# Optimization experiments

Hardware: AMD Instinct MI355X
Metric: run time of the kernel (lower is better)

## Reference

```python
import jax, jax.numpy as jnp
import numpy as np

B, C, T = 128, 8, 128   # batch, channels, time steps
K, S = 20, 128          # known classes, barycenter length


def setup_inputs() -> dict:
    key = jax.random.key(0)
    k1, k2, k3, k4, k5 = jax.random.split(key, 5)
    x = jax.random.normal(k1, (B, C, T), dtype=jnp.float32)
    preds = jax.random.randint(k2, (B,), 0, K).astype(jnp.int32)
    barycenters = jax.random.normal(k3, (K, S, C), dtype=jnp.float32)
    # thresholds centered near realistic scales so both detector branches fire
    top_dist = 7.0 + 0.5 * jax.random.normal(k4, (K,), dtype=jnp.float32)
    bottom_cc = 25.0 + 5.0 * jax.random.normal(k5, (K, C), dtype=jnp.float32)
    return {"x": x, "preds": preds, "barycenters": barycenters,
            "top_dist": top_dist, "bottom_cc": bottom_cc}


def _dtw_dist(cost):
    """Classic DTW DP over a [T, S] sq-euclidean cost matrix; returns accumulated cost."""
    inf = jnp.asarray(jnp.inf, cost.dtype)
    row0 = jnp.cumsum(cost[0])  # first row: only left moves

    def row_step(prev, crow):
        prev_shift = jnp.concatenate([jnp.full((1,), inf, cost.dtype), prev[:-1]])
        def col_step(left, inp):
            c, p, ps = inp
            v = c + jnp.minimum(jnp.minimum(p, ps), left)
            return v, v
        _, row = jax.lax.scan(col_step, inf, (crow, prev, prev_shift))
        return row, None

    last, _ = jax.lax.scan(row_step, row0, cost[1:])
    return last[-1]


def reference(x, preds, barycenters, top_dist, bottom_cc):
    xt = jnp.transpose(x, (0, 2, 1))                    # [B, T, C]
    x2 = jnp.sum(xt * xt, axis=-1)                      # [B, T]
    b2 = jnp.sum(barycenters * barycenters, axis=-1)    # [K, S]
    dots = jnp.einsum('btc,ksc->bkts', xt, barycenters)  # [B, K, T, S]
    cost = jnp.maximum(x2[:, None, :, None] + b2[None, :, None, :] - 2.0 * dots, 0.0)

    Bn, Kn, Tn, Sn = cost.shape
    dists = jax.vmap(_dtw_dist)(cost.reshape(Bn * Kn, Tn, Sn)).reshape(Bn, Kn)
    log_dists = jnp.log(dists)
    dtw_unknown = jnp.all(log_dists > top_dist[None, :], axis=1)   # [B]

    # per-channel full cross-correlation max vs each barycenter
    corr_max = lambda a, v: jnp.max(jnp.correlate(a, v, mode='full'))
    per_ch = jax.vmap(corr_max, in_axes=(1, 1))          # over channels -> [C]
    per_cls = jax.vmap(per_ch, in_axes=(None, 0))        # over classes  -> [K, C]
    per_b = jax.vmap(per_cls, in_axes=(0, None))         # over batch    -> [B, K, C]
    ccs = per_b(xt, barycenters)
    # class 'fails' if any channel cc is not above its bottom threshold
    cc_unknown = jnp.all(jnp.any(ccs <= bottom_cc[None, :, :], axis=2), axis=1)  # [B]

    unknown = cc_unknown | dtw_unknown
    return jnp.where(unknown, Kn, preds)
```

## Files before the change

kernel.cpp:

```cpp
#include <hip/hip_runtime.h>
#include <hip/hip_bf16.h>
#include <math.h>

#define B_ 128
#define C_ 8
#define T_ 128
#define K_ 20
#define S_ 128

__global__ __launch_bounds__(64) void dtw_kernel(const float* __restrict__ x,
                                                 const float* __restrict__ bary,
                                                 const float* __restrict__ top_dist,
                                                 int* __restrict__ dtw_gt) {
    int pair = blockIdx.x;
    int b = pair / K_;
    int kk = pair - b * K_;
    int lane = threadIdx.x;

    __shared__ __align__(16) float xs[T_][C_];

    #pragma unroll
    for (int i = 0; i < (T_ * C_) / 64; ++i) {
        int idx = i * 64 + lane;
        int t = idx & (T_ - 1);
        int c = idx >> 7;
        xs[t][c] = x[(b * C_ + c) * T_ + t];
    }

    float bv0[8], bv1[8];
    {
        const float4* bp = (const float4*)(bary + (size_t)(kk * S_ + 2 * lane) * C_);
        float4 a0 = bp[0], a1 = bp[1], a2 = bp[2], a3 = bp[3];
        bv0[0] = a0.x; bv0[1] = a0.y; bv0[2] = a0.z; bv0[3] = a0.w;
        bv0[4] = a1.x; bv0[5] = a1.y; bv0[6] = a1.z; bv0[7] = a1.w;
        bv1[0] = a2.x; bv1[1] = a2.y; bv1[2] = a2.z; bv1[3] = a2.w;
        bv1[4] = a3.x; bv1[5] = a3.y; bv1[6] = a3.z; bv1[7] = a3.w;
    }
    __syncthreads();

    const float INF = __builtin_inff();
    float c0 = INF, c1 = INF, p0 = INF, p1 = INF;

    for (int d = 0; d < T_ + 63; ++d) {
        float lc = __shfl_up(c1, 1);
        float lp = __shfl_up(p1, 1);
        int t = d - lane;
        if (t >= 0 && t < T_) {
            p0 = c0;
            p1 = c1;
            float4 xa = *(const float4*)&xs[t][0];
            float4 xb = *(const float4*)&xs[t][4];
            float xv[8];
            xv[0] = xa.x; xv[1] = xa.y; xv[2] = xa.z; xv[3] = xa.w;
            xv[4] = xb.x; xv[5] = xb.y; xv[6] = xb.z; xv[7] = xb.w;
            float cost0 = 0.0f, cost1 = 0.0f;
            #pragma unroll
            for (int ch = 0; ch < 8; ++ch) {
                float d0 = xv[ch] - bv0[ch];
                float d1 = xv[ch] - bv1[ch];
                cost0 = fmaf(d0, d0, cost0);
                cost1 = fmaf(d1, d1, cost1);
            }
            float up0 = (t == 0) ? INF : p0;
            float up1 = (t == 0) ? INF : p1;
            float dg1 = (t == 0) ? INF : p0;
            float dg0, lf0;
            if (lane == 0) {
                dg0 = (t == 0) ? 0.0f : INF;
                lf0 = INF;
            } else {
                dg0 = (t == 0) ? INF : lp;
                lf0 = lc;
            }
            c0 = cost0 + fminf(fminf(up0, dg0), lf0);
            c1 = cost1 + fminf(fminf(up1, dg1), c0);
        }
    }

    if (lane == 63) {
        dtw_gt[pair] = (logf(c1) > top_dist[kk]) ? 1 : 0;
    }
}

#define CC_ROW 396

__global__ __launch_bounds__(256) void cc_kernel(const float* __restrict__ x,
                                                 const float* __restrict__ bary,
                                                 const float* __restrict__ bottom_cc,
                                                 int* __restrict__ cc_fail) {
    int pair = blockIdx.x;
    int b = pair / K_;
    int kk = pair - b * K_;
    int tid = threadIdx.x;

    __shared__ __align__(16) float xp[C_ * CC_ROW];
    __shared__ __align__(16) float bt[C_][S_];
    __shared__ int fail;

    if (tid == 0) fail = 0;

    for (int i = tid; i < C_ * CC_ROW; i += 256) {
        int c = i / CC_ROW;
        int j = i - c * CC_ROW;
        int t = j - (S_ - 1);
        float v = 0.0f;
        if (t >= 0 && t < T_) v = x[(b * C_ + c) * T_ + t];
        xp[i] = v;
    }
    for (int i = tid; i < C_ * S_; i += 256) {
        int s = i >> 3;
        int c = i & 7;
        bt[c][s] = bary[(kk * S_ + s) * C_ + c];
    }
    __syncthreads();

    int c = tid >> 5;
    int l = tid & 31;
    int lag0 = l * 8;
    const float* xr = &xp[c * CC_ROW];

    float w[12];
    #pragma unroll
    for (int i = 0; i < 12; i += 4) {
        float4 v4 = *(const float4*)(xr + lag0 + i);
        w[i] = v4.x; w[i + 1] = v4.y; w[i + 2] = v4.z; w[i + 3] = v4.w;
    }
    float acc[8] = {0.f, 0.f, 0.f, 0.f, 0.f, 0.f, 0.f, 0.f};

    for (int s4 = 0; s4 < S_; s4 += 4) {
        #pragma unroll
        for (int u = 0; u < 4; ++u) {
            float bval = bt[c][s4 + u];
            #pragma unroll
            for (int j = 0; j < 8; ++j)
                acc[j] = fmaf(w[u + j], bval, acc[j]);
        }
        #pragma unroll
        for (int i = 0; i < 8; ++i) w[i] = w[i + 4];
        float4 v4 = *(const float4*)(xr + lag0 + s4 + 12);
        w[8] = v4.x; w[9] = v4.y; w[10] = v4.z; w[11] = v4.w;
    }

    if (l == 31) acc[7] = -__builtin_inff();
    float m = acc[0];
    #pragma unroll
    for (int j = 1; j < 8; ++j) m = fmaxf(m, acc[j]);
    #pragma unroll
    for (int off = 16; off > 0; off >>= 1)
        m = fmaxf(m, __shfl_xor(m, off));

    if (l == 0) {
        if (m <= bottom_cc[kk * C_ + c]) atomicOr(&fail, 1);
    }
    __syncthreads();
    if (tid == 0) cc_fail[pair] = fail;
}

__global__ void final_kernel(const int* __restrict__ preds,
                             const int* __restrict__ dtw_gt,
                             const int* __restrict__ cc_fail,
                             int* __restrict__ out) {
    int b = threadIdx.x;
    if (b < B_) {
        int dtw_all = 1, cc_all = 1;
        #pragma unroll
        for (int k = 0; k < K_; ++k) {
            dtw_all &= dtw_gt[b * K_ + k];
            cc_all &= cc_fail[b * K_ + k];
        }
        out[b] = (dtw_all | cc_all) ? K_ : preds[b];
    }
}

extern "C" void kernel_launch(void* const* d_in, const int* in_sizes, int n_in,
                              void* d_out, int out_size, void* d_ws, size_t ws_size,
                              hipStream_t stream) {
    const float* x         = (const float*)d_in[0];
    const int*   preds     = (const int*)d_in[1];
    const float* bary      = (const float*)d_in[2];
    const float* top_dist  = (const float*)d_in[3];
    const float* bottom_cc = (const float*)d_in[4];
    int* out = (int*)d_out;

    int* dtw_gt  = (int*)d_ws;
    int* cc_fail = dtw_gt + B_ * K_;

    dtw_kernel<<<B_ * K_, 64, 0, stream>>>(x, bary, top_dist, dtw_gt);
    cc_kernel<<<B_ * K_, 256, 0, stream>>>(x, bary, bottom_cc, cc_fail);
    final_kernel<<<1, 128, 0, stream>>>(preds, dtw_gt, cc_fail, out);
}
```

Baseline: 65.20 us.

## Fuse DTW and cross-correlation kernels into one interleaved launch

Merges the DTW and cross-correlation kernels into a single 3200-block launch. Every fifth block runs four DTW pairs, one per wave, and the other blocks each run one CC pair, so the two workloads overlap on the GPU and one launch is dropped. The DTW cost is now computed as |x|^2+|b|^2-2x·b using precomputed norms and pre-scaled barycenter values, matching the reference formula. The wavefront loop is simplified with clamped indexing and a carried left-diagonal value, which removes one shuffle per step. The CC inner loop is fully unrolled.

```diff
diff --git a/kernel.cpp b/kernel.cpp
--- a/kernel.cpp
+++ b/kernel.cpp
@@ -8,152 +8,188 @@
 #define K_ 20
 #define S_ 128
 
-__global__ __launch_bounds__(64) void dtw_kernel(const float* __restrict__ x,
-                                                 const float* __restrict__ bary,
-                                                 const float* __restrict__ top_dist,
-                                                 int* __restrict__ dtw_gt) {
-    int pair = blockIdx.x;
-    int b = pair / K_;
-    int kk = pair - b * K_;
-    int lane = threadIdx.x;
-
-    __shared__ __align__(16) float xs[T_][C_];
-
-    #pragma unroll
-    for (int i = 0; i < (T_ * C_) / 64; ++i) {
-        int idx = i * 64 + lane;
-        int t = idx & (T_ - 1);
-        int c = idx >> 7;
-        xs[t][c] = x[(b * C_ + c) * T_ + t];
+#define CC_ROW 396
+#define DTW_TILE_F 1152
+#define SMEM_BYTES 18816
+
+__global__ __launch_bounds__(256) void fused_kernel(const float* __restrict__ x,
+                                                    const float* __restrict__ bary,
+                                                    const float* __restrict__ top_dist,
+                                                    const float* __restrict__ bottom_cc,
+                                                    int* __restrict__ dtw_gt,
+                                                    int* __restrict__ cc_fail) {
+    __shared__ __align__(16) unsigned char smem[SMEM_BYTES];
+    int u = blockIdx.x;
+    int tid = threadIdx.x;
+
+    if (u % 5 == 0) {
+        int wave = tid >> 6;
+        int lane = tid & 63;
+        int pair = (u / 5) * 4 + wave;
+        int b = pair / K_;
+        int kk = pair - b * K_;
+        float* tile = (float*)smem + wave * DTW_TILE_F;
+
+        #pragma unroll
+        for (int i = 0; i < 16; ++i) {
+            int idx = i * 64 + lane;
+            int c = idx >> 7;
+            int t = idx & 127;
+            float v = x[(b * C_ + c) * T_ + t];
+            tile[t * 4 + (c & 3) + ((c >> 2) * 512)] = v;
+        }
+        __syncthreads();
+        #pragma unroll
+        for (int rep = 0; rep < 2; ++rep) {
+            int t = rep * 64 + lane;
+            float4 xa = *(const float4*)&tile[t * 4];
+            float4 xb = *(const float4*)&tile[512 + t * 4];
+            float s = xa.x * xa.x;
+            s = fmaf(xa.y, xa.y, s); s = fmaf(xa.z, xa.z, s); s = fmaf(xa.w, xa.w, s);
+            s = fmaf(xb.x, xb.x, s); s = fmaf(xb.y, xb.y, s); s = fmaf(xb.z, xb.z, s);
+            s = fmaf(xb.w, xb.w, s);
+            tile[1024 + t] = s;
+        }
+        __syncthreads();
+
+        float bv0[8], bv1[8], B20, B21;
+        {
+            const float4* bp = (const float4*)(bary + (size_t)(kk * S_ + 2 * lane) * C_);
+            float4 q0 = bp[0], q1 = bp[1], q2 = bp[2], q3 = bp[3];
+            bv0[0]=q0.x; bv0[1]=q0.y; bv0[2]=q0.z; bv0[3]=q0.w;
+            bv0[4]=q1.x; bv0[5]=q1.y; bv0[6]=q1.z; bv0[7]=q1.w;
+            bv1[0]=q2.x; bv1[1]=q2.y; bv1[2]=q2.z; bv1[3]=q2.w;
+            bv1[4]=q3.x; bv1[5]=q3.y; bv1[6]=q3.z; bv1[7]=q3.w;
+            float s0 = 0.f, s1 = 0.f;
+            #pragma unroll
+            for (int ch = 0; ch < 8; ++ch) {
+                s0 = fmaf(bv0[ch], bv0[ch], s0);
+                s1 = fmaf(bv1[ch], bv1[ch], s1);
+            }
+            B20 = s0; B21 = s1;
+            #pragma unroll
+            for (int ch = 0; ch < 8; ++ch) { bv0[ch] *= -2.f; bv1[ch] *= -2.f; }
+        }
+
+        const float INF = __builtin_inff();
+        float c0 = INF, c1 = INF, lcp = INF;
+        bool is0 = (lane == 0);
+
+        if (is0) {
+            float bse = tile[1024];
+            float4 xa = *(const float4*)&tile[0];
+            float4 xb = *(const float4*)&tile[512];
+            float a0 = bse + B20, a1 = bse + B21;
+            a0 = fmaf(bv0[0], xa.x, a0); a0 = fmaf(bv0[1], xa.y, a0);
+            a0 = fmaf(bv0[2], xa.z, a0); a0 = fmaf(bv0[3], xa.w, a0);
+            a0 = fmaf(bv0[4], xb.x, a0); a0 = fmaf(bv0[5], xb.y, a0);
+            a0 = fmaf(bv0[6], xb.z, a0); a0 = fmaf(bv0[7], xb.w, a0);
+            a1 = fmaf(bv1[0], xa.x, a1); a1 = fmaf(bv1[1], xa.y, a1);
+            a1 = fmaf(bv1[2], xa.z, a1); a1 = fmaf(bv1[3], xa.w, a1);
+            a1 = fmaf(bv1[4], xb.x, a1); a1 = fmaf(bv1[5], xb.y, a1);
+            a1 = fmaf(bv1[6], xb.z, a1); a1 = fmaf(bv1[7], xb.w, a1);
+            c0 = fmaxf(a0, 0.f);
+            c1 = fmaxf(a1, 0.f) + c0;
+        }
+
+        for (int d = 1; d < T_ + 63; ++d) {
+            float lcs = __shfl_up(c1, 1);
+            float lc = is0 ? INF : lcs;
+            int t = d - lane;
+            if (t >= 0) {
+                int tc = (t < 127) ? t : 127;
+                float bse = tile[1024 + tc];
+                float4 xa = *(const float4*)&tile[tc * 4];
+                float4 xb = *(const float4*)&tile[512 + tc * 4];
+                float a0 = bse + B20, a1 = bse + B21;
+                a0 = fmaf(bv0[0], xa.x, a0); a0 = fmaf(bv0[1], xa.y, a0);
+                a0 = fmaf(bv0[2], xa.z, a0); a0 = fmaf(bv0[3], xa.w, a0);
+                a0 = fmaf(bv0[4], xb.x, a0); a0 = fmaf(bv0[5], xb.y, a0);
+                a0 = fmaf(bv0[6], xb.z, a0); a0 = fmaf(bv0[7], xb.w, a0);
+                a1 = fmaf(bv1[0], xa.x, a1); a1 = fmaf(bv1[1], xa.y, a1);
+                a1 = fmaf(bv1[2], xa.z, a1); a1 = fmaf(bv1[3], xa.w, a1);
+                a1 = fmaf(bv1[4], xb.x, a1); a1 = fmaf(bv1[5], xb.y, a1);
+                a1 = fmaf(bv1[6], xb.z, a1); a1 = fmaf(bv1[7], xb.w, a1);
+                a0 = fmaxf(a0, 0.f);
+                a1 = fmaxf(a1, 0.f);
+                float n0 = a0 + fminf(fminf(c0, lcp), lc);
+                float n1 = a1 + fminf(fminf(c1, c0), n0);
+                c0 = n0; c1 = n1;
+            }
+            lcp = lc;
+        }
+
+        if (lane == 63)
+            dtw_gt[pair] = (logf(c1) > top_dist[kk]) ? 1 : 0;
+    } else {
+        int pair = u - (u + 4) / 5;
+        int b = pair / K_;
+        int kk = pair - b * K_;
+
+        float* xp = (float*)smem;
+        float* bt = xp + C_ * CC_ROW;
+        int* fail = (int*)(bt + C_ * S_);
+
+        if (tid == 0) *fail = 0;
+
+        for (int i = tid; i < C_ * CC_ROW; i += 256) {
+            int c = i / CC_ROW;
+            int j = i - c * CC_ROW;
+            int t = j - (S_ - 1);
+            float v = 0.0f;
+            if (t >= 0 && t < T_) v = x[(b * C_ + c) * T_ + t];
+            xp[i] = v;
+        }
+        for (int i = tid; i < C_ * S_; i += 256) {
+            int s = i >> 3;
+            int c = i & 7;
+            bt[c * S_ + s] = bary[(kk * S_ + s) * C_ + c];
+        }
+        __syncthreads();
+
+        int c = tid >> 5;
+        int l = tid & 31;
+        int lag0 = l * 8;
+        const float* xr = &xp[c * CC_ROW];
+        const float* br = &bt[c * S_];
+
+        float w[12];
+        #pragma unroll
+        for (int i = 0; i < 12; i += 4) {
+            float4 v4 = *(const float4*)(xr + lag0 + i);
+            w[i] = v4.x; w[i+1] = v4.y; w[i+2] = v4.z; w[i+3] = v4.w;
+        }
+        float acc[8] = {0.f,0.f,0.f,0.f,0.f,0.f,0.f,0.f};
+
+        #pragma unroll
+        for (int s4 = 0; s4 < S_; s4 += 4) {
+            #pragma unroll
+            for (int uu = 0; uu < 4; ++uu) {
+                float bval = br[s4 + uu];
+                #pragma unroll
+                for (int j = 0; j < 8; ++j)
+                    acc[j] = fmaf(w[uu + j], bval, acc[j]);
+            }
+            #pragma unroll
+            for (int i = 0; i < 8; ++i) w[i] = w[i + 4];
+            float4 v4 = *(const float4*)(xr + lag0 + s4 + 12);
+            w[8] = v4.x; w[9] = v4.y; w[10] = v4.z; w[11] = v4.w;
+        }
+
+        if (l == 31) acc[7] = -__builtin_inff();
+        float m = acc[0];
+        #pragma unroll
+        for (int j = 1; j < 8; ++j) m = fmaxf(m, acc[j]);
+        #pragma unroll
+        for (int off = 16; off > 0; off >>= 1)
+            m = fmaxf(m, __shfl_xor(m, off));
+
+        if (l == 0) {
+            if (m <= bottom_cc[kk * C_ + c]) atomicOr(fail, 1);
+        }
+        __syncthreads();
+        if (tid == 0) cc_fail[pair] = *fail;
     }
-
-    float bv0[8], bv1[8];
-    {
-        const float4* bp = (const float4*)(bary + (size_t)(kk * S_ + 2 * lane) * C_);
-        float4 a0 = bp[0], a1 = bp[1], a2 = bp[2], a3 = bp[3];
-        bv0[0] = a0.x; bv0[1] = a0.y; bv0[2] = a0.z; bv0[3] = a0.w;
-        bv0[4] = a1.x; bv0[5] = a1.y; bv0[6] = a1.z; bv0[7] = a1.w;
-        bv1[0] = a2.x; bv1[1] = a2.y; bv1[2] = a2.z; bv1[3] = a2.w;
-        bv1[4] = a3.x; bv1[5] = a3.y; bv1[6] = a3.z; bv1[7] = a3.w;
-    }
-    __syncthreads();
-
-    const float INF = __builtin_inff();
-    float c0 = INF, c1 = INF, p0 = INF, p1 = INF;
-
-    for (int d = 0; d < T_ + 63; ++d) {
-        float lc = __shfl_up(c1, 1);
-        float lp = __shfl_up(p1, 1);
-        int t = d - lane;
-        if (t >= 0 && t < T_) {
-            p0 = c0;
-            p1 = c1;
-            float4 xa = *(const float4*)&xs[t][0];
-            float4 xb = *(const float4*)&xs[t][4];
-            float xv[8];
-            xv[0] = xa.x; xv[1] = xa.y; xv[2] = xa.z; xv[3] = xa.w;
-            xv[4] = xb.x; xv[5] = xb.y; xv[6] = xb.z; xv[7] = xb.w;
-            float cost0 = 0.0f, cost1 = 0.0f;
-            #pragma unroll
-            for (int ch = 0; ch < 8; ++ch) {
-                float d0 = xv[ch] - bv0[ch];
-                float d1 = xv[ch] - bv1[ch];
-                cost0 = fmaf(d0, d0, cost0);
-                cost1 = fmaf(d1, d1, cost1);
-            }
-            float up0 = (t == 0) ? INF : p0;
-            float up1 = (t == 0) ? INF : p1;
-            float dg1 = (t == 0) ? INF : p0;
-            float dg0, lf0;
-            if (lane == 0) {
-                dg0 = (t == 0) ? 0.0f : INF;
-                lf0 = INF;
-            } else {
-                dg0 = (t == 0) ? INF : lp;
-                lf0 = lc;
-            }
-            c0 = cost0 + fminf(fminf(up0, dg0), lf0);
-            c1 = cost1 + fminf(fminf(up1, dg1), c0);
-        }
-    }
-
-    if (lane == 63) {
-        dtw_gt[pair] = (logf(c1) > top_dist[kk]) ? 1 : 0;
-    }
-}
-
-#define CC_ROW 396
-
-__global__ __launch_bounds__(256) void cc_kernel(const float* __restrict__ x,
-                                                 const float* __restrict__ bary,
-                                                 const float* __restrict__ bottom_cc,
-                                                 int* __restrict__ cc_fail) {
-    int pair = blockIdx.x;
-    int b = pair / K_;
-    int kk = pair - b * K_;
-    int tid = threadIdx.x;
-
-    __shared__ __align__(16) float xp[C_ * CC_ROW];
-    __shared__ __align__(16) float bt[C_][S_];
-    __shared__ int fail;
-
-    if (tid == 0) fail = 0;
-
-    for (int i = tid; i < C_ * CC_ROW; i += 256) {
-        int c = i / CC_ROW;
-        int j = i - c * CC_ROW;
-        int t = j - (S_ - 1);
-        float v = 0.0f;
-        if (t >= 0 && t < T_) v = x[(b * C_ + c) * T_ + t];
-        xp[i] = v;
-    }
-    for (int i = tid; i < C_ * S_; i += 256) {
-        int s = i >> 3;
-        int c = i & 7;
-        bt[c][s] = bary[(kk * S_ + s) * C_ + c];
-    }
-    __syncthreads();
-
-    int c = tid >> 5;
-    int l = tid & 31;
-    int lag0 = l * 8;
-    const float* xr = &xp[c * CC_ROW];
-
-    float w[12];
-    #pragma unroll
-    for (int i = 0; i < 12; i += 4) {
-        float4 v4 = *(const float4*)(xr + lag0 + i);
-        w[i] = v4.x; w[i + 1] = v4.y; w[i + 2] = v4.z; w[i + 3] = v4.w;
-    }
-    float acc[8] = {0.f, 0.f, 0.f, 0.f, 0.f, 0.f, 0.f, 0.f};
-
-    for (int s4 = 0; s4 < S_; s4 += 4) {
-        #pragma unroll
-        for (int u = 0; u < 4; ++u) {
-            float bval = bt[c][s4 + u];
-            #pragma unroll
-            for (int j = 0; j < 8; ++j)
-                acc[j] = fmaf(w[u + j], bval, acc[j]);
-        }
-        #pragma unroll
-        for (int i = 0; i < 8; ++i) w[i] = w[i + 4];
-        float4 v4 = *(const float4*)(xr + lag0 + s4 + 12);
-        w[8] = v4.x; w[9] = v4.y; w[10] = v4.z; w[11] = v4.w;
-    }
-
-    if (l == 31) acc[7] = -__builtin_inff();
-    float m = acc[0];
-    #pragma unroll
-    for (int j = 1; j < 8; ++j) m = fmaxf(m, acc[j]);
-    #pragma unroll
-    for (int off = 16; off > 0; off >>= 1)
-        m = fmaxf(m, __shfl_xor(m, off));
-
-    if (l == 0) {
-        if (m <= bottom_cc[kk * C_ + c]) atomicOr(&fail, 1);
-    }
-    __syncthreads();
-    if (tid == 0) cc_fail[pair] = fail;
 }
 
 __global__ void final_kernel(const int* __restrict__ preds,
@@ -185,7 +221,6 @@
     int* dtw_gt  = (int*)d_ws;
     int* cc_fail = dtw_gt + B_ * K_;
 
-    dtw_kernel<<<B_ * K_, 64, 0, stream>>>(x, bary, top_dist, dtw_gt);
-    cc_kernel<<<B_ * K_, 256, 0, stream>>>(x, bary, bottom_cc, cc_fail);
+    fused_kernel<<<3200, 256, 0, stream>>>(x, bary, top_dist, bottom_cc, dtw_gt, cc_fail);
     final_kernel<<<1, 128, 0, stream>>>(preds, dtw_gt, cc_fail, out);
 }
```

New measurement: 76.09 us. 1.17x slower.

## Fuse DTW and cross-correlation into one interleaved heterogeneous-block kernel

Applied to the files above, without the earlier changes.

Merges the DTW and cross-correlation kernels into a single launch of 6400 single-wave blocks. One in five blocks runs DTW for two classes using 32 lanes each with four columns per lane, which shortens the wavefront diagonal. The DTW cost is computed from precomputed norms plus a dot product. The remaining blocks each handle half the channels of a (batch, class) pair for cross-correlation, with a 16-lag register window and a swizzled shared layout. The intent is to overlap the latency-bound DTW chains with FMA-heavy correlation work and to cut launch overhead, at the cost of more registers and uneven block durations.

```diff
diff --git a/kernel.cpp b/kernel.cpp
--- a/kernel.cpp
+++ b/kernel.cpp
@@ -8,157 +8,188 @@
 #define K_ 20
 #define S_ 128
 
-__global__ __launch_bounds__(64) void dtw_kernel(const float* __restrict__ x,
-                                                 const float* __restrict__ bary,
-                                                 const float* __restrict__ top_dist,
-                                                 int* __restrict__ dtw_gt) {
-    int pair = blockIdx.x;
-    int b = pair / K_;
-    int kk = pair - b * K_;
+#define XROW 384
+#define BTROW 132
+#define SWZ(j) ((j) ^ ((((j) >> 5) & 7) << 2))
+#define SMEMF 2080
+
+__global__ __launch_bounds__(64) void fused_kernel(const float* __restrict__ x,
+                                                   const float* __restrict__ bary,
+                                                   const float* __restrict__ top_dist,
+                                                   const float* __restrict__ bottom_cc,
+                                                   int* __restrict__ dtw_gt,
+                                                   int* __restrict__ cc_fail2) {
+    __shared__ __align__(16) float smem[SMEMF];
+    const float INF = __builtin_inff();
+    int u = blockIdx.x;
     int lane = threadIdx.x;
 
-    __shared__ __align__(16) float xs[T_][C_];
-
-    #pragma unroll
-    for (int i = 0; i < (T_ * C_) / 64; ++i) {
-        int idx = i * 64 + lane;
-        int t = idx & (T_ - 1);
-        int c = idx >> 7;
-        xs[t][c] = x[(b * C_ + c) * T_ + t];
-    }
-
-    float bv0[8], bv1[8];
-    {
-        const float4* bp = (const float4*)(bary + (size_t)(kk * S_ + 2 * lane) * C_);
-        float4 a0 = bp[0], a1 = bp[1], a2 = bp[2], a3 = bp[3];
-        bv0[0] = a0.x; bv0[1] = a0.y; bv0[2] = a0.z; bv0[3] = a0.w;
-        bv0[4] = a1.x; bv0[5] = a1.y; bv0[6] = a1.z; bv0[7] = a1.w;
-        bv1[0] = a2.x; bv1[1] = a2.y; bv1[2] = a2.z; bv1[3] = a2.w;
-        bv1[4] = a3.x; bv1[5] = a3.y; bv1[6] = a3.z; bv1[7] = a3.w;
-    }
-    __syncthreads();
-
-    const float INF = __builtin_inff();
-    float c0 = INF, c1 = INF, p0 = INF, p1 = INF;
-
-    for (int d = 0; d < T_ + 63; ++d) {
-        float lc = __shfl_up(c1, 1);
-        float lp = __shfl_up(p1, 1);
-        int t = d - lane;
-        if (t >= 0 && t < T_) {
-            p0 = c0;
-            p1 = c1;
-            float4 xa = *(const float4*)&xs[t][0];
-            float4 xb = *(const float4*)&xs[t][4];
-            float xv[8];
-            xv[0] = xa.x; xv[1] = xa.y; xv[2] = xa.z; xv[3] = xa.w;
-            xv[4] = xb.x; xv[5] = xb.y; xv[6] = xb.z; xv[7] = xb.w;
-            float cost0 = 0.0f, cost1 = 0.0f;
+    if (u % 5 == 0) {
+        int w = u / 5;
+        int b = w / 10;
+        int j2 = w - b * 10;
+        int gl = lane & 31;
+        int kk = j2 * 2 + (lane >> 5);
+
+        #pragma unroll
+        for (int i = 0; i < 4; ++i) {
+            int vid = i * 64 + lane;
+            int c = vid >> 5;
+            int t0 = (vid & 31) << 2;
+            float4 v = *(const float4*)(x + ((size_t)b * C_ + c) * T_ + t0);
+            float* dst = &smem[(c >> 2) * 512 + (c & 3)];
+            dst[(t0 + 0) * 4] = v.x;
+            dst[(t0 + 1) * 4] = v.y;
+            dst[(t0 + 2) * 4] = v.z;
+            dst[(t0 + 3) * 4] = v.w;
+        }
+        __syncthreads();
+        #pragma unroll
+        for (int r = 0; r < 2; ++r) {
+            int t = r * 64 + lane;
+            float4 xa = *(const float4*)&smem[t * 4];
+            float4 xb = *(const float4*)&smem[512 + t * 4];
+            float s = xa.x * xa.x;
+            s = fmaf(xa.y, xa.y, s); s = fmaf(xa.z, xa.z, s); s = fmaf(xa.w, xa.w, s);
+            s = fmaf(xb.x, xb.x, s); s = fmaf(xb.y, xb.y, s); s = fmaf(xb.z, xb.z, s);
+            s = fmaf(xb.w, xb.w, s);
+            smem[1024 + t] = s;
+        }
+        __syncthreads();
+
+        float bv[4][8], B2s[4];
+        {
+            const float4* bp = (const float4*)(bary + ((size_t)kk * S_ + 4 * gl) * C_);
             #pragma unroll
-            for (int ch = 0; ch < 8; ++ch) {
-                float d0 = xv[ch] - bv0[ch];
-                float d1 = xv[ch] - bv1[ch];
-                cost0 = fmaf(d0, d0, cost0);
-                cost1 = fmaf(d1, d1, cost1);
-            }
-            float up0 = (t == 0) ? INF : p0;
-            float up1 = (t == 0) ? INF : p1;
-            float dg1 = (t == 0) ? INF : p0;
-            float dg0, lf0;
-            if (lane == 0) {
-                dg0 = (t == 0) ? 0.0f : INF;
-                lf0 = INF;
-            } else {
-                dg0 = (t == 0) ? INF : lp;
-                lf0 = lc;
-            }
-            c0 = cost0 + fminf(fminf(up0, dg0), lf0);
-            c1 = cost1 + fminf(fminf(up1, dg1), c0);
-        }
-    }
-
-    if (lane == 63) {
-        dtw_gt[pair] = (logf(c1) > top_dist[kk]) ? 1 : 0;
+            for (int r = 0; r < 4; ++r) {
+                float4 q0 = bp[2 * r], q1 = bp[2 * r + 1];
+                bv[r][0] = q0.x; bv[r][1] = q0.y; bv[r][2] = q0.z; bv[r][3] = q0.w;
+                bv[r][4] = q1.x; bv[r][5] = q1.y; bv[r][6] = q1.z; bv[r][7] = q1.w;
+                float s = 0.f;
+                #pragma unroll
+                for (int ch = 0; ch < 8; ++ch) s = fmaf(bv[r][ch], bv[r][ch], s);
+                B2s[r] = s;
+                #pragma unroll
+                for (int ch = 0; ch < 8; ++ch) bv[r][ch] *= -2.f;
+            }
+        }
+
+        bool is0 = (gl == 0);
+        float cr0 = INF, cr1 = INF, cr2 = INF, cr3 = INF;
+        float lcp = is0 ? 0.f : INF;
+
+        for (int d = 0; d < T_ + 31; ++d) {
+            float lcs = __shfl_up(cr3, 1);
+            float lc = is0 ? INF : lcs;
+            int t = d - gl;
+            if (t >= 0) {
+                int tc = (t < T_ - 1) ? t : (T_ - 1);
+                float bse = smem[1024 + tc];
+                float4 xa = *(const float4*)&smem[tc * 4];
+                float4 xb = *(const float4*)&smem[512 + tc * 4];
+                float xv[8];
+                xv[0] = xa.x; xv[1] = xa.y; xv[2] = xa.z; xv[3] = xa.w;
+                xv[4] = xb.x; xv[5] = xb.y; xv[6] = xb.z; xv[7] = xb.w;
+                float a0 = bse + B2s[0], a1 = bse + B2s[1];
+                float a2 = bse + B2s[2], a3 = bse + B2s[3];
+                #pragma unroll
+                for (int ch = 0; ch < 8; ++ch) {
+                    a0 = fmaf(bv[0][ch], xv[ch], a0);
+                    a1 = fmaf(bv[1][ch], xv[ch], a1);
+                    a2 = fmaf(bv[2][ch], xv[ch], a2);
+                    a3 = fmaf(bv[3][ch], xv[ch], a3);
+                }
+                a0 = fmaxf(a0, 0.f); a1 = fmaxf(a1, 0.f);
+                a2 = fmaxf(a2, 0.f); a3 = fmaxf(a3, 0.f);
+                float n0 = a0 + fminf(fminf(cr0, lcp), lc);
+                float n1 = a1 + fminf(fminf(cr1, cr0), n0);
+                float n2 = a2 + fminf(fminf(cr2, cr1), n1);
+                float n3 = a3 + fminf(fminf(cr3, cr2), n2);
+                cr0 = n0; cr1 = n1; cr2 = n2; cr3 = n3;
+            }
+            lcp = lc;
+        }
+
+        if (gl == 31)
+            dtw_gt[b * K_ + kk] = (logf(cr3) > top_dist[kk]) ? 1 : 0;
+    } else {
+        int idx = u - u / 5 - 1;
+        int pair = idx >> 1;
+        int h = idx & 1;
+        int b = pair / K_;
+        int kk = pair - b * K_;
+        int cbase = h * 4;
+
+        float* xp = smem;
+        float* bt = smem + 4 * XROW;
+
+        #pragma unroll
+        for (int c = 0; c < 4; ++c)
+            for (int j = lane; j < XROW; j += 64) {
+                int t = j - (S_ - 1);
+                float v = 0.f;
+                if (t >= 0 && t < T_) v = x[((size_t)b * C_ + cbase + c) * T_ + t];
+                xp[c * XROW + SWZ(j)] = v;
+            }
+        for (int i = lane; i < 4 * S_; i += 64) {
+            int s = i >> 2, c = i & 3;
+            bt[c * BTROW + s] = bary[((size_t)kk * S_ + s) * C_ + cbase + c];
+        }
+        __syncthreads();
+
+        int cl = lane >> 4;
+        int gl = lane & 15;
+        int lag0 = gl << 4;
+        const float* xr = xp + cl * XROW;
+        const float* br = bt + cl * BTROW;
+
+        float wdw[20];
+        #pragma unroll
+        for (int i = 0; i < 5; ++i) {
+            float4 v = *(const float4*)&xr[SWZ(lag0 + i * 4)];
+            wdw[i * 4 + 0] = v.x; wdw[i * 4 + 1] = v.y;
+            wdw[i * 4 + 2] = v.z; wdw[i * 4 + 3] = v.w;
+        }
+        float acc[16];
+        #pragma unroll
+        for (int j = 0; j < 16; ++j) acc[j] = 0.f;
+
+        #pragma unroll
+        for (int s4 = 0; s4 < S_; s4 += 4) {
+            float4 bq = *(const float4*)&br[s4];
+            float bvals[4] = {bq.x, bq.y, bq.z, bq.w};
+            #pragma unroll
+            for (int uu = 0; uu < 4; ++uu) {
+                #pragma unroll
+                for (int j = 0; j < 16; ++j)
+                    acc[j] = fmaf(wdw[uu + j], bvals[uu], acc[j]);
+            }
+            if (s4 < S_ - 4) {
+                #pragma unroll
+                for (int i = 0; i < 16; ++i) wdw[i] = wdw[i + 4];
+                float4 v = *(const float4*)&xr[SWZ(lag0 + s4 + 20)];
+                wdw[16] = v.x; wdw[17] = v.y; wdw[18] = v.z; wdw[19] = v.w;
+            }
+        }
+
+        if (gl == 15) acc[15] = -INF;
+        float m = acc[0];
+        #pragma unroll
+        for (int j = 1; j < 16; ++j) m = fmaxf(m, acc[j]);
+        #pragma unroll
+        for (int off = 8; off >= 1; off >>= 1)
+            m = fmaxf(m, __shfl_xor(m, off));
+
+        bool fail = false;
+        if (gl == 0) fail = (m <= bottom_cc[kk * C_ + cbase + cl]);
+        unsigned long long bal = __ballot(fail);
+        if (lane == 0) cc_fail2[pair * 2 + h] = (bal != 0ULL) ? 1 : 0;
     }
 }
 
-#define CC_ROW 396
-
-__global__ __launch_bounds__(256) void cc_kernel(const float* __restrict__ x,
-                                                 const float* __restrict__ bary,
-                                                 const float* __restrict__ bottom_cc,
-                                                 int* __restrict__ cc_fail) {
-    int pair = blockIdx.x;
-    int b = pair / K_;
-    int kk = pair - b * K_;
-    int tid = threadIdx.x;
-
-    __shared__ __align__(16) float xp[C_ * CC_ROW];
-    __shared__ __align__(16) float bt[C_][S_];
-    __shared__ int fail;
-
-    if (tid == 0) fail = 0;
-
-    for (int i = tid; i < C_ * CC_ROW; i += 256) {
-        int c = i / CC_ROW;
-        int j = i - c * CC_ROW;
-        int t = j - (S_ - 1);
-        float v = 0.0f;
-        if (t >= 0 && t < T_) v = x[(b * C_ + c) * T_ + t];
-        xp[i] = v;
-    }
-    for (int i = tid; i < C_ * S_; i += 256) {
-        int s = i >> 3;
-        int c = i & 7;
-        bt[c][s] = bary[(kk * S_ + s) * C_ + c];
-    }
-    __syncthreads();
-
-    int c = tid >> 5;
-    int l = tid & 31;
-    int lag0 = l * 8;
-    const float* xr = &xp[c * CC_ROW];
-
-    float w[12];
-    #pragma unroll
-    for (int i = 0; i < 12; i += 4) {
-        float4 v4 = *(const float4*)(xr + lag0 + i);
-        w[i] = v4.x; w[i + 1] = v4.y; w[i + 2] = v4.z; w[i + 3] = v4.w;
-    }
-    float acc[8] = {0.f, 0.f, 0.f, 0.f, 0.f, 0.f, 0.f, 0.f};
-
-    for (int s4 = 0; s4 < S_; s4 += 4) {
-        #pragma unroll
-        for (int u = 0; u < 4; ++u) {
-            float bval = bt[c][s4 + u];
-            #pragma unroll
-            for (int j = 0; j < 8; ++j)
-                acc[j] = fmaf(w[u + j], bval, acc[j]);
-        }
-        #pragma unroll
-        for (int i = 0; i < 8; ++i) w[i] = w[i + 4];
-        float4 v4 = *(const float4*)(xr + lag0 + s4 + 12);
-        w[8] = v4.x; w[9] = v4.y; w[10] = v4.z; w[11] = v4.w;
-    }
-
-    if (l == 31) acc[7] = -__builtin_inff();
-    float m = acc[0];
-    #pragma unroll
-    for (int j = 1; j < 8; ++j) m = fmaxf(m, acc[j]);
-    #pragma unroll
-    for (int off = 16; off > 0; off >>= 1)
-        m = fmaxf(m, __shfl_xor(m, off));
-
-    if (l == 0) {
-        if (m <= bottom_cc[kk * C_ + c]) atomicOr(&fail, 1);
-    }
-    __syncthreads();
-    if (tid == 0) cc_fail[pair] = fail;
-}
-
 __global__ void final_kernel(const int* __restrict__ preds,
                              const int* __restrict__ dtw_gt,
-                             const int* __restrict__ cc_fail,
+                             const int* __restrict__ cc_fail2,
                              int* __restrict__ out) {
     int b = threadIdx.x;
     if (b < B_) {
@@ -166,7 +197,7 @@
         #pragma unroll
         for (int k = 0; k < K_; ++k) {
             dtw_all &= dtw_gt[b * K_ + k];
-            cc_all &= cc_fail[b * K_ + k];
+            cc_all &= (cc_fail2[(b * K_ + k) * 2] | cc_fail2[(b * K_ + k) * 2 + 1]);
         }
         out[b] = (dtw_all | cc_all) ? K_ : preds[b];
     }
@@ -182,10 +213,9 @@
     const float* bottom_cc = (const float*)d_in[4];
     int* out = (int*)d_out;
 
-    int* dtw_gt  = (int*)d_ws;
-    int* cc_fail = dtw_gt + B_ * K_;
-
-    dtw_kernel<<<B_ * K_, 64, 0, stream>>>(x, bary, top_dist, dtw_gt);
-    cc_kernel<<<B_ * K_, 256, 0, stream>>>(x, bary, bottom_cc, cc_fail);
-    final_kernel<<<1, 128, 0, stream>>>(preds, dtw_gt, cc_fail, out);
+    int* dtw_gt   = (int*)d_ws;
+    int* cc_fail2 = dtw_gt + B_ * K_;
+
+    fused_kernel<<<6400, 64, 0, stream>>>(x, bary, top_dist, bottom_cc, dtw_gt, cc_fail2);
+    final_kernel<<<1, 128, 0, stream>>>(preds, dtw_gt, cc_fail2, out);
 }
```

Result: no change. 65.11 us (-0.1%).
